# Performance work log

Measured on AMD Instinct MI355X. Metric: run time of the kernel, lower is better.

The kernel has to match this reference:

```python
import jax, jax.numpy as jnp
import numpy as np

# Production-scale dims
B = 256        # graphs per batch
NPG = 500      # nodes per graph (equal-size graphs; k<=NPG so no padding branch)
N = B * NPG    # 128000 total nodes
F = 128        # num_node_feats
D = 32         # latent_dim
K = 30         # sort-pool k
L = 3          # num_layers
E = 2_048_000  # edges (avg degree 16)


def _mlp(x, wa, ba, wb, bb):
    # 2-layer MLP(in -> D -> D) with ReLU between layers (standard GIN-style MLP)
    return jax.nn.relu(x @ wa + ba) @ wb + bb


def setup_inputs() -> dict:
    key = jax.random.key(0)
    ks = jax.random.split(key, 10)
    s = 0.05
    return {
        "node_feat": jax.random.normal(ks[0], (N, F), jnp.float32),
        "alpha": jax.random.normal(ks[1], (L + 1,), jnp.float32) * 0.5,
        "w0a": jax.random.normal(ks[2], (F, D), jnp.float32) * s,
        "b0a": jnp.zeros((D,), jnp.float32),
        "w0b": jax.random.normal(ks[3], (D, D), jnp.float32) * s,
        "b0b": jnp.zeros((D,), jnp.float32),
        "W1a": jax.random.normal(ks[4], (L, 3 * D, D), jnp.float32) * s,
        "B1a": jnp.zeros((L, D), jnp.float32),
        "W1b": jax.random.normal(ks[5], (L, D, D), jnp.float32) * s,
        "B1b": jnp.zeros((L, D), jnp.float32),
        "edge_src": jax.random.randint(ks[6], (E,), 0, N, jnp.int32),
        "edge_dst": jax.random.randint(ks[7], (E,), 0, N, jnp.int32),
    }


def reference(node_feat, alpha, w0a, b0a, w0b, b0b, W1a, B1a, W1b, B1b,
              edge_src, edge_dst):
    # --- aggregate_combine ---
    ego = _mlp(node_feat, w0a, b0a, w0b, b0b)            # [N, D]
    out = alpha[0] * ego
    for l in range(L):
        # gnn_spmm(n2n_sp, ego): binary adjacency SpMM == scatter-add over edges
        neig = jax.ops.segment_sum(ego[edge_src], edge_dst, num_segments=N)  # [N, D]
        agg = jnp.concatenate([ego, neig, neig + ego], axis=1)               # [N, 3D]
        ego = _mlp(agg, W1a[l], B1a[l], W1b[l], B1b[l])                      # [N, D]
        out = out + alpha[l + 1] * ego
    # --- per-graph sort pooling on wl_color = last channel of final ego ---
    wl_color = ego[:, -1].reshape(B, NPG)                # [B, NPG]
    _, idx = jax.lax.top_k(wl_color, K)                  # [B, K] local indices
    gidx = (idx + jnp.arange(B, dtype=idx.dtype)[:, None] * NPG).reshape(-1)
    sort_graphs = out[gidx].reshape(B, K * D)            # [B, k*latent_dim]
    return jax.nn.relu(sort_graphs)
```

## Files before the change

kernel.cpp:

```cpp
#include <hip/hip_runtime.h>
#include <math.h>

#define N_NODES 128000
#define B_G 256
#define NPG 500
#define F_IN 128
#define D_LAT 32
#define K_TOP 30
#define L_LAYERS 3
#define E_EDGES 2048000

#define BSH 7
#define NB (N_NODES >> BSH)
#define CHUNK 8192
#define CBLOCKS (E_EDGES / CHUNK)

__global__ __launch_bounds__(256) void k_foldw(
    const float* __restrict__ W1a, float* __restrict__ wfold)
{
    const int l = blockIdx.x, t = threadIdx.x;
    const float* base = W1a + (size_t)l * 3 * D_LAT * D_LAT;
    float* o = wfold + (size_t)l * 2 * D_LAT * D_LAT;
    for (int i = t; i < D_LAT * D_LAT; i += 256) {
        const float wc = base[2 * D_LAT * D_LAT + i];
        o[i] = base[i] + wc;
        o[D_LAT * D_LAT + i] = base[D_LAT * D_LAT + i] + wc;
    }
}

__global__ __launch_bounds__(256) void k_mlp0(
    const float* __restrict__ X, const float* __restrict__ w0a,
    const float* __restrict__ b0a, const float* __restrict__ w0b,
    const float* __restrict__ b0b, const float* __restrict__ alpha,
    float* __restrict__ ego, float* __restrict__ outb)
{
    const size_t row = (size_t)blockIdx.x * 256 + threadIdx.x;
    const float4* xp = (const float4*)(X + row * F_IN);
    const float a0 = alpha[0];

    float acc[D_LAT];
    #pragma unroll
    for (int j = 0; j < D_LAT; ++j) acc[j] = b0a[j];

    #pragma unroll 1
    for (int c = 0; c < F_IN / 16; ++c) {
        const float4 x0 = xp[c * 4 + 0], x1 = xp[c * 4 + 1];
        const float4 x2 = xp[c * 4 + 2], x3 = xp[c * 4 + 3];
        const float xs[16] = {x0.x, x0.y, x0.z, x0.w, x1.x, x1.y, x1.z, x1.w,
                              x2.x, x2.y, x2.z, x2.w, x3.x, x3.y, x3.z, x3.w};
        #pragma unroll
        for (int ff = 0; ff < 16; ++ff) {
            const float xf = xs[ff];
            const float* wr = w0a + (c * 16 + ff) * D_LAT;
            #pragma unroll
            for (int j = 0; j < D_LAT; ++j)
                acc[j] = fmaf(xf, wr[j], acc[j]);
        }
    }

    #pragma unroll
    for (int j = 0; j < D_LAT; ++j) acc[j] = fmaxf(acc[j], 0.f);

    float acc2[D_LAT];
    #pragma unroll
    for (int j = 0; j < D_LAT; ++j) acc2[j] = b0b[j];
    #pragma unroll 1
    for (int c = 0; c < D_LAT / 8; ++c) {
        #pragma unroll
        for (int kk = 0; kk < 8; ++kk) {
            const float h = acc[c * 8 + kk];
            const float* wr = w0b + (c * 8 + kk) * D_LAT;
            #pragma unroll
            for (int j = 0; j < D_LAT; ++j)
                acc2[j] = fmaf(h, wr[j], acc2[j]);
        }
    }

    float4* eo = (float4*)(ego + row * D_LAT);
    float4* oo = (float4*)(outb + row * D_LAT);
    #pragma unroll
    for (int q = 0; q < D_LAT / 4; ++q) {
        eo[q] = make_float4(acc2[q*4], acc2[q*4+1], acc2[q*4+2], acc2[q*4+3]);
        oo[q] = make_float4(a0*acc2[q*4], a0*acc2[q*4+1],
                            a0*acc2[q*4+2], a0*acc2[q*4+3]);
    }
}

__global__ __launch_bounds__(256) void k_bcount(
    const int* __restrict__ edst, int* __restrict__ ghist)
{
    __shared__ int cnt[NB];
    const int t = threadIdx.x;
    for (int i = t; i < NB; i += 256) cnt[i] = 0;
    __syncthreads();
    const int ebase = blockIdx.x * CHUNK;
    for (int i = 0; i < CHUNK / 256; ++i)
        atomicAdd(&cnt[edst[ebase + i * 256 + t] >> BSH], 1);
    __syncthreads();
    for (int i = t; i < NB; i += 256)
        if (cnt[i]) atomicAdd(&ghist[i], cnt[i]);
}

__global__ __launch_bounds__(1024) void k_bscan(
    const int* __restrict__ ghist, int* __restrict__ gbase,
    int* __restrict__ gcursor)
{
    __shared__ int buf[2][1024];
    const int t = threadIdx.x;
    const int v = (t < NB) ? ghist[t] : 0;
    buf[0][t] = v;
    __syncthreads();
    int cur = 0;
    for (int o = 1; o < 1024; o <<= 1) {
        int x = buf[cur][t];
        if (t >= o) x += buf[cur][t - o];
        buf[cur ^ 1][t] = x;
        cur ^= 1;
        __syncthreads();
    }
    if (t < NB) { const int e = buf[cur][t] - v; gbase[t] = e; gcursor[t] = e; }
    if (t == 0) gbase[NB] = E_EDGES;
}

__global__ __launch_bounds__(256) void k_bscatter(
    const int* __restrict__ esrc, const int* __restrict__ edst,
    int* __restrict__ gcursor, int* __restrict__ packed)
{
    __shared__ int cnt[NB];
    __shared__ int sbase[NB];
    const int t = threadIdx.x;
    for (int i = t; i < NB; i += 256) cnt[i] = 0;
    __syncthreads();
    const int ebase = blockIdx.x * CHUNK;
    for (int i = 0; i < CHUNK / 256; ++i)
        atomicAdd(&cnt[edst[ebase + i * 256 + t] >> BSH], 1);
    __syncthreads();
    for (int i = t; i < NB; i += 256) {
        const int c = cnt[i];
        sbase[i] = c ? atomicAdd(&gcursor[i], c) : 0;
        cnt[i] = 0;
    }
    __syncthreads();
    for (int i = 0; i < CHUNK / 256; ++i) {
        const int e = ebase + i * 256 + t;
        const int d = edst[e], s = esrc[e];
        const int b = d >> BSH;
        const int r = atomicAdd(&cnt[b], 1);
        packed[sbase[b] + r] = (s << BSH) | (d & ((1 << BSH) - 1));
    }
}

__global__ __launch_bounds__(256) void k_bcsr(
    const int* __restrict__ gbase, const int* __restrict__ packed,
    int* __restrict__ off, int* __restrict__ srcidx)
{
    __shared__ int cnt[128];
    __shared__ int scn[128];
    __shared__ int sbuf[4096];
    const int b = blockIdx.x, t = threadIdx.x;
    const int s0 = gbase[b], s1 = gbase[b + 1], m = s1 - s0;

    if (t < 128) cnt[t] = 0;
    __syncthreads();
    for (int i = t; i < m; i += 256)
        atomicAdd(&cnt[packed[s0 + i] & 127], 1);
    __syncthreads();
    if (t == 0) {
        int a = 0;
        for (int k = 0; k < 128; ++k) { scn[k] = a; a += cnt[k]; }
    }
    __syncthreads();
    if (t < 128) { off[(b << BSH) + t] = s0 + scn[t]; cnt[t] = 0; }
    if (b == 0 && t == 0) off[N_NODES] = E_EDGES;
    __syncthreads();
    for (int i = t; i < m; i += 256) {
        const int p = packed[s0 + i];
        const int dl = p & 127;
        const int r = atomicAdd(&cnt[dl], 1);
        sbuf[scn[dl] + r] = p >> BSH;
    }
    __syncthreads();
    for (int i = t; i < m; i += 256) srcidx[s0 + i] = sbuf[i];
}

__global__ __launch_bounds__(256) void k_layer(
    const float* __restrict__ in, const int* __restrict__ off,
    const int* __restrict__ srcidx, const float* __restrict__ wfold_l,
    const float* __restrict__ W1b_l, const float* __restrict__ B1a_l,
    const float* __restrict__ B1b_l, const float* __restrict__ alpha,
    const int l, float* __restrict__ out, float* __restrict__ outb)
{
    const size_t n = (size_t)blockIdx.x * 256 + threadIdx.x;
    const int s0 = off[n], s1 = off[n + 1];
    const float al = alpha[l + 1];

    float4 ng4[D_LAT / 4];
    #pragma unroll
    for (int q = 0; q < D_LAT / 4; ++q) ng4[q] = make_float4(0.f, 0.f, 0.f, 0.f);
    int s = (s0 < s1) ? srcidx[s0] : 0;
    for (int i = s0; i < s1; ++i) {
        const int snext = (i + 1 < s1) ? srcidx[i + 1] : 0;
        const float4* vp = (const float4*)(in + (size_t)s * D_LAT);
        #pragma unroll
        for (int q = 0; q < D_LAT / 4; ++q) {
            const float4 v = vp[q];
            ng4[q].x += v.x; ng4[q].y += v.y; ng4[q].z += v.z; ng4[q].w += v.w;
        }
        s = snext;
    }
    float ngs[D_LAT];
    #pragma unroll
    for (int q = 0; q < D_LAT / 4; ++q) {
        ngs[q*4] = ng4[q].x; ngs[q*4+1] = ng4[q].y;
        ngs[q*4+2] = ng4[q].z; ngs[q*4+3] = ng4[q].w;
    }

    float eg[D_LAT];
    {
        const float4* ep = (const float4*)(in + n * D_LAT);
        #pragma unroll
        for (int q = 0; q < D_LAT / 4; ++q) {
            const float4 v = ep[q];
            eg[q*4] = v.x; eg[q*4+1] = v.y; eg[q*4+2] = v.z; eg[q*4+3] = v.w;
        }
    }

    float acc[D_LAT];
    #pragma unroll
    for (int j = 0; j < D_LAT; ++j) acc[j] = B1a_l[j];
    #pragma unroll 1
    for (int c = 0; c < D_LAT / 8; ++c) {
        #pragma unroll
        for (int kk = 0; kk < 8; ++kk) {
            const int k = c * 8 + kk;
            const float fe = eg[k], fn = ngs[k];
            const float* we = wfold_l + k * D_LAT;
            const float* wn = wfold_l + D_LAT * D_LAT + k * D_LAT;
            #pragma unroll
            for (int j = 0; j < D_LAT; ++j)
                acc[j] = fmaf(fe, we[j], fmaf(fn, wn[j], acc[j]));
        }
    }
    #pragma unroll
    for (int j = 0; j < D_LAT; ++j) acc[j] = fmaxf(acc[j], 0.f);

    float acc2[D_LAT];
    #pragma unroll
    for (int j = 0; j < D_LAT; ++j) acc2[j] = B1b_l[j];
    #pragma unroll 1
    for (int c = 0; c < D_LAT / 8; ++c) {
        #pragma unroll
        for (int kk = 0; kk < 8; ++kk) {
            const float h = acc[c * 8 + kk];
            const float* wr = W1b_l + (c * 8 + kk) * D_LAT;
            #pragma unroll
            for (int j = 0; j < D_LAT; ++j)
                acc2[j] = fmaf(h, wr[j], acc2[j]);
        }
    }

    float4* eo = (float4*)(out + n * D_LAT);
    float4* oo = (float4*)(outb + n * D_LAT);
    #pragma unroll
    for (int q = 0; q < D_LAT / 4; ++q) {
        const float4 prev = oo[q];
        eo[q] = make_float4(acc2[q*4], acc2[q*4+1], acc2[q*4+2], acc2[q*4+3]);
        oo[q] = make_float4(fmaf(al, acc2[q*4], prev.x),
                            fmaf(al, acc2[q*4+1], prev.y),
                            fmaf(al, acc2[q*4+2], prev.z),
                            fmaf(al, acc2[q*4+3], prev.w));
    }
}

__global__ __launch_bounds__(256) void k_topk(
    const float* __restrict__ ego, const float* __restrict__ outb,
    float* __restrict__ y)
{
    __shared__ float vals[512];
    __shared__ int topidx[K_TOP];
    __shared__ float wv[4];
    __shared__ int wi[4];

    const int g = blockIdx.x, t = threadIdx.x;
    for (int i = t; i < 512; i += 256)
        vals[i] = (i < NPG) ? ego[((size_t)g * NPG + i) * D_LAT + (D_LAT - 1)]
                            : -INFINITY;
    __syncthreads();

    for (int k = 0; k < K_TOP; ++k) {
        float v = -INFINITY; int bi = 0x7fffffff;
        for (int i = t; i < NPG; i += 256) {
            const float x = vals[i];
            if (x > v || (x == v && i < bi)) { v = x; bi = i; }
        }
        for (int off = 32; off > 0; off >>= 1) {
            const float ov = __shfl_down(v, off);
            const int   oi = __shfl_down(bi, off);
            if (ov > v || (ov == v && oi < bi)) { v = ov; bi = oi; }
        }
        if ((t & 63) == 0) { wv[t >> 6] = v; wi[t >> 6] = bi; }
        __syncthreads();
        if (t == 0) {
            for (int w = 1; w < 4; ++w)
                if (wv[w] > v || (wv[w] == v && wi[w] < bi)) { v = wv[w]; bi = wi[w]; }
            topidx[k] = bi;
            vals[bi] = -INFINITY;
        }
        __syncthreads();
    }

    for (int j = t; j < K_TOP * D_LAT; j += 256) {
        const int kk = j >> 5, d = j & 31;
        const size_t node = (size_t)g * NPG + topidx[kk];
        y[(size_t)g * (K_TOP * D_LAT) + j] = fmaxf(outb[node * D_LAT + d], 0.f);
    }
}

extern "C" void kernel_launch(void* const* d_in, const int* in_sizes, int n_in,
                              void* d_out, int out_size, void* d_ws, size_t ws_size,
                              hipStream_t stream)
{
    const float* X    = (const float*)d_in[0];
    const float* alpha= (const float*)d_in[1];
    const float* w0a  = (const float*)d_in[2];
    const float* b0a  = (const float*)d_in[3];
    const float* w0b  = (const float*)d_in[4];
    const float* b0b  = (const float*)d_in[5];
    const float* W1a  = (const float*)d_in[6];
    const float* B1a  = (const float*)d_in[7];
    const float* W1b  = (const float*)d_in[8];
    const float* B1b  = (const float*)d_in[9];
    const int* esrc   = (const int*)d_in[10];
    const int* edst   = (const int*)d_in[11];
    float* y = (float*)d_out;

    float* egoA   = (float*)d_ws;
    float* outb   = egoA + (size_t)N_NODES * D_LAT;
    float* egoB   = outb + (size_t)N_NODES * D_LAT;
    int*   packed = (int*)egoB;
    int*   off    = (int*)(egoB + (size_t)N_NODES * D_LAT);
    int*   srcidx = off + (N_NODES + 1);
    int*   ghist  = srcidx + E_EDGES;
    int*   gbase  = ghist + NB;
    int*   gcursor= gbase + (NB + 1);
    float* wfold  = (float*)(gcursor + NB);

    k_foldw<<<L_LAYERS, 256, 0, stream>>>(W1a, wfold);

    hipMemsetAsync(ghist, 0, NB * sizeof(int), stream);
    k_bcount  <<<CBLOCKS, 256, 0, stream>>>(edst, ghist);
    k_bscan   <<<1, 1024, 0, stream>>>(ghist, gbase, gcursor);
    k_bscatter<<<CBLOCKS, 256, 0, stream>>>(esrc, edst, gcursor, packed);
    k_bcsr    <<<NB, 256, 0, stream>>>(gbase, packed, off, srcidx);

    k_mlp0<<<N_NODES / 256, 256, 0, stream>>>(X, w0a, b0a, w0b, b0b, alpha, egoA, outb);

    float* cur = egoA;
    float* nxt = egoB;
    for (int l = 0; l < L_LAYERS; ++l) {
        k_layer<<<N_NODES / 256, 256, 0, stream>>>(
            cur, off, srcidx, wfold + (size_t)l * 2 * D_LAT * D_LAT,
            W1b + (size_t)l * D_LAT * D_LAT, B1a + (size_t)l * D_LAT,
            B1b + (size_t)l * D_LAT, alpha, l, nxt, outb);
        float* tmp = cur; cur = nxt; nxt = tmp;
    }

    k_topk<<<B_G, 256, 0, stream>>>(cur, outb, y);
}
```

Measured before the change: 430.8 us.

## Split each node's gather across two lanes and exchange halves via shuffles

Each node in the layer kernel is now handled by two threads. Each thread gathers and accumulates half of the 32 neighbour features, and the gather loop is unrolled by two so more loads are in flight. The halves are swapped with xor-shuffles so both threads hold the full vectors, then each writes its own half of the output. The aim is more memory-level parallelism and occupancy for the irregular gather. The cost is that both threads repeat the full 32x32 MLP, doubling that compute.

```diff
diff --git a/kernel.cpp b/kernel.cpp
--- a/kernel.cpp
+++ b/kernel.cpp
@@ -190,39 +190,61 @@
     const float* __restrict__ B1b_l, const float* __restrict__ alpha,
     const int l, float* __restrict__ out, float* __restrict__ outb)
 {
-    const size_t n = (size_t)blockIdx.x * 256 + threadIdx.x;
+    const int gtid = blockIdx.x * 256 + threadIdx.x;
+    const size_t n = (size_t)(gtid >> 1);
+    const int half = gtid & 1;
     const int s0 = off[n], s1 = off[n + 1];
     const float al = alpha[l + 1];
 
-    float4 ng4[D_LAT / 4];
-    #pragma unroll
-    for (int q = 0; q < D_LAT / 4; ++q) ng4[q] = make_float4(0.f, 0.f, 0.f, 0.f);
-    int s = (s0 < s1) ? srcidx[s0] : 0;
-    for (int i = s0; i < s1; ++i) {
-        const int snext = (i + 1 < s1) ? srcidx[i + 1] : 0;
-        const float4* vp = (const float4*)(in + (size_t)s * D_LAT);
-        #pragma unroll
-        for (int q = 0; q < D_LAT / 4; ++q) {
-            const float4 v = vp[q];
-            ng4[q].x += v.x; ng4[q].y += v.y; ng4[q].z += v.z; ng4[q].w += v.w;
-        }
-        s = snext;
-    }
-    float ngs[D_LAT];
-    #pragma unroll
-    for (int q = 0; q < D_LAT / 4; ++q) {
-        ngs[q*4] = ng4[q].x; ngs[q*4+1] = ng4[q].y;
-        ngs[q*4+2] = ng4[q].z; ngs[q*4+3] = ng4[q].w;
-    }
-
-    float eg[D_LAT];
+    const float* inh = in + half * 16;
+
+    float4 g0 = {0,0,0,0}, g1 = {0,0,0,0}, g2 = {0,0,0,0}, g3 = {0,0,0,0};
+    int i = s0;
+    for (; i + 2 <= s1; i += 2) {
+        const int sa = srcidx[i], sb = srcidx[i + 1];
+        const float4* pa = (const float4*)(inh + (size_t)sa * D_LAT);
+        const float4* pb = (const float4*)(inh + (size_t)sb * D_LAT);
+        const float4 a0 = pa[0], a1 = pa[1], a2 = pa[2], a3 = pa[3];
+        const float4 b0 = pb[0], b1 = pb[1], b2 = pb[2], b3 = pb[3];
+        g0.x += a0.x + b0.x; g0.y += a0.y + b0.y; g0.z += a0.z + b0.z; g0.w += a0.w + b0.w;
+        g1.x += a1.x + b1.x; g1.y += a1.y + b1.y; g1.z += a1.z + b1.z; g1.w += a1.w + b1.w;
+        g2.x += a2.x + b2.x; g2.y += a2.y + b2.y; g2.z += a2.z + b2.z; g2.w += a2.w + b2.w;
+        g3.x += a3.x + b3.x; g3.y += a3.y + b3.y; g3.z += a3.z + b3.z; g3.w += a3.w + b3.w;
+    }
+    if (i < s1) {
+        const int sa = srcidx[i];
+        const float4* pa = (const float4*)(inh + (size_t)sa * D_LAT);
+        const float4 a0 = pa[0], a1 = pa[1], a2 = pa[2], a3 = pa[3];
+        g0.x += a0.x; g0.y += a0.y; g0.z += a0.z; g0.w += a0.w;
+        g1.x += a1.x; g1.y += a1.y; g1.z += a1.z; g1.w += a1.w;
+        g2.x += a2.x; g2.y += a2.y; g2.z += a2.z; g2.w += a2.w;
+        g3.x += a3.x; g3.y += a3.y; g3.z += a3.z; g3.w += a3.w;
+    }
+    float mine[16];
+    mine[0]=g0.x; mine[1]=g0.y; mine[2]=g0.z; mine[3]=g0.w;
+    mine[4]=g1.x; mine[5]=g1.y; mine[6]=g1.z; mine[7]=g1.w;
+    mine[8]=g2.x; mine[9]=g2.y; mine[10]=g2.z; mine[11]=g2.w;
+    mine[12]=g3.x; mine[13]=g3.y; mine[14]=g3.z; mine[15]=g3.w;
+
+    float emine[16];
     {
-        const float4* ep = (const float4*)(in + n * D_LAT);
-        #pragma unroll
-        for (int q = 0; q < D_LAT / 4; ++q) {
-            const float4 v = ep[q];
-            eg[q*4] = v.x; eg[q*4+1] = v.y; eg[q*4+2] = v.z; eg[q*4+3] = v.w;
-        }
+        const float4* ep = (const float4*)(inh + n * D_LAT);
+        const float4 e0 = ep[0], e1 = ep[1], e2 = ep[2], e3 = ep[3];
+        emine[0]=e0.x; emine[1]=e0.y; emine[2]=e0.z; emine[3]=e0.w;
+        emine[4]=e1.x; emine[5]=e1.y; emine[6]=e1.z; emine[7]=e1.w;
+        emine[8]=e2.x; emine[9]=e2.y; emine[10]=e2.z; emine[11]=e2.w;
+        emine[12]=e3.x; emine[13]=e3.y; emine[14]=e3.z; emine[15]=e3.w;
+    }
+
+    float ngs[D_LAT], eg[D_LAT];
+    #pragma unroll
+    for (int d = 0; d < 16; ++d) {
+        const float og = __shfl_xor(mine[d], 1);
+        const float oe = __shfl_xor(emine[d], 1);
+        ngs[d]      = half ? og       : mine[d];
+        ngs[16 + d] = half ? mine[d]  : og;
+        eg[d]       = half ? oe       : emine[d];
+        eg[16 + d]  = half ? emine[d] : oe;
     }
 
     float acc[D_LAT];
@@ -259,16 +281,18 @@
         }
     }
 
-    float4* eo = (float4*)(out + n * D_LAT);
-    float4* oo = (float4*)(outb + n * D_LAT);
-    #pragma unroll
-    for (int q = 0; q < D_LAT / 4; ++q) {
+    float4* eo = (float4*)(out + n * D_LAT + half * 16);
+    float4* oo = (float4*)(outb + n * D_LAT + half * 16);
+    #pragma unroll
+    for (int q = 0; q < 4; ++q) {
+        const float v0 = half ? acc2[16 + q*4 + 0] : acc2[q*4 + 0];
+        const float v1 = half ? acc2[16 + q*4 + 1] : acc2[q*4 + 1];
+        const float v2 = half ? acc2[16 + q*4 + 2] : acc2[q*4 + 2];
+        const float v3 = half ? acc2[16 + q*4 + 3] : acc2[q*4 + 3];
         const float4 prev = oo[q];
-        eo[q] = make_float4(acc2[q*4], acc2[q*4+1], acc2[q*4+2], acc2[q*4+3]);
-        oo[q] = make_float4(fmaf(al, acc2[q*4], prev.x),
-                            fmaf(al, acc2[q*4+1], prev.y),
-                            fmaf(al, acc2[q*4+2], prev.z),
-                            fmaf(al, acc2[q*4+3], prev.w));
+        eo[q] = make_float4(v0, v1, v2, v3);
+        oo[q] = make_float4(fmaf(al, v0, prev.x), fmaf(al, v1, prev.y),
+                            fmaf(al, v2, prev.z), fmaf(al, v3, prev.w));
     }
 }
 
@@ -358,7 +382,7 @@
     float* cur = egoA;
     float* nxt = egoB;
     for (int l = 0; l < L_LAYERS; ++l) {
-        k_layer<<<N_NODES / 256, 256, 0, stream>>>(
+        k_layer<<<N_NODES * 2 / 256, 256, 0, stream>>>(
             cur, off, srcidx, wfold + (size_t)l * 2 * D_LAT * D_LAT,
             W1b + (size_t)l * D_LAT * D_LAT, B1a + (size_t)l * D_LAT,
             B1b + (size_t)l * D_LAT, alpha, l, nxt, outb);
```

After: 878.1 us. +103.8%, slower.

## Split each node's neighbor gather across two lanes with shuffle reduction

Applied to the files above, without the earlier changes.

Each node in the layer kernel is now handled by two threads, each summing alternate incoming edges, and the partial neighbor sums are combined with a cross-lane shuffle. Both lanes then redundantly compute the full 2-layer MLP, and the two output stores are divided between them. This doubles memory-level parallelism in the latency-bound gather and halves per-thread serial edge traversal, at the cost of duplicating the MLP FLOPs, doubling thread count, and dropping the previous software prefetch of the next source index.

```diff
diff --git a/kernel.cpp b/kernel.cpp
--- a/kernel.cpp
+++ b/kernel.cpp
@@ -190,36 +190,39 @@
     const float* __restrict__ B1b_l, const float* __restrict__ alpha,
     const int l, float* __restrict__ out, float* __restrict__ outb)
 {
-    const size_t n = (size_t)blockIdx.x * 256 + threadIdx.x;
+    const int gtid = blockIdx.x * 256 + threadIdx.x;
+    const size_t n = (size_t)(gtid >> 1);
+    const int half = gtid & 1;
     const int s0 = off[n], s1 = off[n + 1];
     const float al = alpha[l + 1];
 
-    float4 ng4[D_LAT / 4];
-    #pragma unroll
-    for (int q = 0; q < D_LAT / 4; ++q) ng4[q] = make_float4(0.f, 0.f, 0.f, 0.f);
-    int s = (s0 < s1) ? srcidx[s0] : 0;
-    for (int i = s0; i < s1; ++i) {
-        const int snext = (i + 1 < s1) ? srcidx[i + 1] : 0;
+    float4 ng[8];
+    #pragma unroll
+    for (int q = 0; q < 8; ++q) ng[q] = make_float4(0.f, 0.f, 0.f, 0.f);
+    for (int i = s0 + half; i < s1; i += 2) {
+        const int s = srcidx[i];
         const float4* vp = (const float4*)(in + (size_t)s * D_LAT);
         #pragma unroll
-        for (int q = 0; q < D_LAT / 4; ++q) {
+        for (int q = 0; q < 8; ++q) {
             const float4 v = vp[q];
-            ng4[q].x += v.x; ng4[q].y += v.y; ng4[q].z += v.z; ng4[q].w += v.w;
-        }
-        s = snext;
-    }
+            ng[q].x += v.x; ng[q].y += v.y; ng[q].z += v.z; ng[q].w += v.w;
+        }
+    }
+
     float ngs[D_LAT];
     #pragma unroll
-    for (int q = 0; q < D_LAT / 4; ++q) {
-        ngs[q*4] = ng4[q].x; ngs[q*4+1] = ng4[q].y;
-        ngs[q*4+2] = ng4[q].z; ngs[q*4+3] = ng4[q].w;
+    for (int q = 0; q < 8; ++q) {
+        ngs[q*4+0] = ng[q].x + __shfl_xor(ng[q].x, 1);
+        ngs[q*4+1] = ng[q].y + __shfl_xor(ng[q].y, 1);
+        ngs[q*4+2] = ng[q].z + __shfl_xor(ng[q].z, 1);
+        ngs[q*4+3] = ng[q].w + __shfl_xor(ng[q].w, 1);
     }
 
     float eg[D_LAT];
     {
         const float4* ep = (const float4*)(in + n * D_LAT);
         #pragma unroll
-        for (int q = 0; q < D_LAT / 4; ++q) {
+        for (int q = 0; q < 8; ++q) {
             const float4 v = ep[q];
             eg[q*4] = v.x; eg[q*4+1] = v.y; eg[q*4+2] = v.z; eg[q*4+3] = v.w;
         }
@@ -259,16 +262,21 @@
         }
     }
 
-    float4* eo = (float4*)(out + n * D_LAT);
-    float4* oo = (float4*)(outb + n * D_LAT);
-    #pragma unroll
-    for (int q = 0; q < D_LAT / 4; ++q) {
-        const float4 prev = oo[q];
-        eo[q] = make_float4(acc2[q*4], acc2[q*4+1], acc2[q*4+2], acc2[q*4+3]);
-        oo[q] = make_float4(fmaf(al, acc2[q*4], prev.x),
-                            fmaf(al, acc2[q*4+1], prev.y),
-                            fmaf(al, acc2[q*4+2], prev.z),
-                            fmaf(al, acc2[q*4+3], prev.w));
+    if (half == 0) {
+        float4* eo = (float4*)(out + n * D_LAT);
+        #pragma unroll
+        for (int q = 0; q < 8; ++q)
+            eo[q] = make_float4(acc2[q*4], acc2[q*4+1], acc2[q*4+2], acc2[q*4+3]);
+    } else {
+        float4* oo = (float4*)(outb + n * D_LAT);
+        #pragma unroll
+        for (int q = 0; q < 8; ++q) {
+            const float4 prev = oo[q];
+            oo[q] = make_float4(fmaf(al, acc2[q*4], prev.x),
+                                fmaf(al, acc2[q*4+1], prev.y),
+                                fmaf(al, acc2[q*4+2], prev.z),
+                                fmaf(al, acc2[q*4+3], prev.w));
+        }
     }
 }
 
@@ -358,7 +366,7 @@
     float* cur = egoA;
     float* nxt = egoB;
     for (int l = 0; l < L_LAYERS; ++l) {
-        k_layer<<<N_NODES / 256, 256, 0, stream>>>(
+        k_layer<<<N_NODES * 2 / 256, 256, 0, stream>>>(
             cur, off, srcidx, wfold + (size_t)l * 2 * D_LAT * D_LAT,
             W1b + (size_t)l * D_LAT * D_LAT, B1a + (size_t)l * D_LAT,
             B1b + (size_t)l * D_LAT, alpha, l, nxt, outb);
```

Result: slower. 467.9 us (+8.6%).

## Split each node across 8 lanes in layer kernel with shuffle-based MLP

Applied to the files above, without the earlier changes.

The layer kernel now assigns 8 threads per node, each owning a float4 slice of the 32-wide feature vector. Neighbor gathers become coalesced 128-byte row reads across the 8 lanes. The two small matmuls broadcast inputs with warp shuffles instead of each thread holding full 32-element arrays. This cuts register pressure, raises occupancy and improves gather coalescing, at the cost of many shuffles and a grid eight times larger.

```diff
diff --git a/kernel.cpp b/kernel.cpp
--- a/kernel.cpp
+++ b/kernel.cpp
@@ -190,86 +190,59 @@
     const float* __restrict__ B1b_l, const float* __restrict__ alpha,
     const int l, float* __restrict__ out, float* __restrict__ outb)
 {
-    const size_t n = (size_t)blockIdx.x * 256 + threadIdx.x;
+    const int t = threadIdx.x;
+    const int lj = t & 7;
+    const int c0 = lj * 4;
+    const int gbase = t & 56;
+    const size_t n = (size_t)blockIdx.x * 32 + (t >> 3);
     const int s0 = off[n], s1 = off[n + 1];
     const float al = alpha[l + 1];
 
-    float4 ng4[D_LAT / 4];
-    #pragma unroll
-    for (int q = 0; q < D_LAT / 4; ++q) ng4[q] = make_float4(0.f, 0.f, 0.f, 0.f);
-    int s = (s0 < s1) ? srcidx[s0] : 0;
+    float4 ng = make_float4(0.f, 0.f, 0.f, 0.f);
     for (int i = s0; i < s1; ++i) {
-        const int snext = (i + 1 < s1) ? srcidx[i + 1] : 0;
-        const float4* vp = (const float4*)(in + (size_t)s * D_LAT);
-        #pragma unroll
-        for (int q = 0; q < D_LAT / 4; ++q) {
-            const float4 v = vp[q];
-            ng4[q].x += v.x; ng4[q].y += v.y; ng4[q].z += v.z; ng4[q].w += v.w;
-        }
-        s = snext;
-    }
-    float ngs[D_LAT];
-    #pragma unroll
-    for (int q = 0; q < D_LAT / 4; ++q) {
-        ngs[q*4] = ng4[q].x; ngs[q*4+1] = ng4[q].y;
-        ngs[q*4+2] = ng4[q].z; ngs[q*4+3] = ng4[q].w;
-    }
-
-    float eg[D_LAT];
-    {
-        const float4* ep = (const float4*)(in + n * D_LAT);
-        #pragma unroll
-        for (int q = 0; q < D_LAT / 4; ++q) {
-            const float4 v = ep[q];
-            eg[q*4] = v.x; eg[q*4+1] = v.y; eg[q*4+2] = v.z; eg[q*4+3] = v.w;
-        }
-    }
-
-    float acc[D_LAT];
-    #pragma unroll
-    for (int j = 0; j < D_LAT; ++j) acc[j] = B1a_l[j];
-    #pragma unroll 1
-    for (int c = 0; c < D_LAT / 8; ++c) {
-        #pragma unroll
-        for (int kk = 0; kk < 8; ++kk) {
-            const int k = c * 8 + kk;
-            const float fe = eg[k], fn = ngs[k];
-            const float* we = wfold_l + k * D_LAT;
-            const float* wn = wfold_l + D_LAT * D_LAT + k * D_LAT;
-            #pragma unroll
-            for (int j = 0; j < D_LAT; ++j)
-                acc[j] = fmaf(fe, we[j], fmaf(fn, wn[j], acc[j]));
-        }
-    }
-    #pragma unroll
-    for (int j = 0; j < D_LAT; ++j) acc[j] = fmaxf(acc[j], 0.f);
-
-    float acc2[D_LAT];
-    #pragma unroll
-    for (int j = 0; j < D_LAT; ++j) acc2[j] = B1b_l[j];
-    #pragma unroll 1
-    for (int c = 0; c < D_LAT / 8; ++c) {
-        #pragma unroll
-        for (int kk = 0; kk < 8; ++kk) {
-            const float h = acc[c * 8 + kk];
-            const float* wr = W1b_l + (c * 8 + kk) * D_LAT;
-            #pragma unroll
-            for (int j = 0; j < D_LAT; ++j)
-                acc2[j] = fmaf(h, wr[j], acc2[j]);
-        }
-    }
-
-    float4* eo = (float4*)(out + n * D_LAT);
-    float4* oo = (float4*)(outb + n * D_LAT);
-    #pragma unroll
-    for (int q = 0; q < D_LAT / 4; ++q) {
-        const float4 prev = oo[q];
-        eo[q] = make_float4(acc2[q*4], acc2[q*4+1], acc2[q*4+2], acc2[q*4+3]);
-        oo[q] = make_float4(fmaf(al, acc2[q*4], prev.x),
-                            fmaf(al, acc2[q*4+1], prev.y),
-                            fmaf(al, acc2[q*4+2], prev.z),
-                            fmaf(al, acc2[q*4+3], prev.w));
-    }
+        const int s = srcidx[i];
+        const float4 v = *(const float4*)(in + (size_t)s * D_LAT + c0);
+        ng.x += v.x; ng.y += v.y; ng.z += v.z; ng.w += v.w;
+    }
+    const float4 e4 = *(const float4*)(in + n * D_LAT + c0);
+
+    float a0 = B1a_l[c0], a1 = B1a_l[c0+1], a2 = B1a_l[c0+2], a3 = B1a_l[c0+3];
+    #pragma unroll
+    for (int k = 0; k < D_LAT; ++k) {
+        const int src = gbase | (k >> 2);
+        const float ec = (k&3)==0 ? e4.x : (k&3)==1 ? e4.y : (k&3)==2 ? e4.z : e4.w;
+        const float nc = (k&3)==0 ? ng.x : (k&3)==1 ? ng.y : (k&3)==2 ? ng.z : ng.w;
+        const float fe = __shfl(ec, src);
+        const float fn = __shfl(nc, src);
+        const float4 we = *(const float4*)(wfold_l + k * D_LAT + c0);
+        const float4 wn = *(const float4*)(wfold_l + D_LAT * D_LAT + k * D_LAT + c0);
+        a0 = fmaf(fe, we.x, fmaf(fn, wn.x, a0));
+        a1 = fmaf(fe, we.y, fmaf(fn, wn.y, a1));
+        a2 = fmaf(fe, we.z, fmaf(fn, wn.z, a2));
+        a3 = fmaf(fe, we.w, fmaf(fn, wn.w, a3));
+    }
+    a0 = fmaxf(a0, 0.f); a1 = fmaxf(a1, 0.f);
+    a2 = fmaxf(a2, 0.f); a3 = fmaxf(a3, 0.f);
+
+    float b0 = B1b_l[c0], b1 = B1b_l[c0+1], b2 = B1b_l[c0+2], b3 = B1b_l[c0+3];
+    #pragma unroll
+    for (int k = 0; k < D_LAT; ++k) {
+        const int src = gbase | (k >> 2);
+        const float hc = (k&3)==0 ? a0 : (k&3)==1 ? a1 : (k&3)==2 ? a2 : a3;
+        const float h = __shfl(hc, src);
+        const float4 w = *(const float4*)(W1b_l + k * D_LAT + c0);
+        b0 = fmaf(h, w.x, b0);
+        b1 = fmaf(h, w.y, b1);
+        b2 = fmaf(h, w.z, b2);
+        b3 = fmaf(h, w.w, b3);
+    }
+
+    float4* eo = (float4*)(out + n * D_LAT + c0);
+    float4* oo = (float4*)(outb + n * D_LAT + c0);
+    const float4 prev = *oo;
+    *eo = make_float4(b0, b1, b2, b3);
+    *oo = make_float4(fmaf(al, b0, prev.x), fmaf(al, b1, prev.y),
+                      fmaf(al, b2, prev.z), fmaf(al, b3, prev.w));
 }
 
 __global__ __launch_bounds__(256) void k_topk(
@@ -358,7 +331,7 @@
     float* cur = egoA;
     float* nxt = egoB;
     for (int l = 0; l < L_LAYERS; ++l) {
-        k_layer<<<N_NODES / 256, 256, 0, stream>>>(
+        k_layer<<<N_NODES / 32, 256, 0, stream>>>(
             cur, off, srcidx, wfold + (size_t)l * 2 * D_LAT * D_LAT,
             W1b + (size_t)l * D_LAT * D_LAT, B1a + (size_t)l * D_LAT,
             B1b + (size_t)l * D_LAT, alpha, l, nxt, outb);
```

Result: slower. 540.5 us (+25.4%).
